# Kernel optimization log

Measured on AMD Instinct MI355X. Metric: run time of the kernel, lower is better.

## Reference

```python
import jax, jax.numpy as jnp
import numpy as np

B = 65536
N_PTS = 11        # n_trajectory_points
N_NEWTON = 5      # shooting_max_iter (fixed-count Newton shooting)
METRIC_FLOOR = 0.1


def _metric(c, lam, W1, b1, W2, b2, W3, b3):
    # g(c, lambda) > 0 ; c, lam: [B]
    x = jnp.stack([c, lam], axis=-1)              # [B, 2]
    h = jnp.tanh(x @ W1 + b1)
    h = jnp.tanh(h @ W2 + b2)
    return jax.nn.softplus((h @ W3 + b3)[..., 0]) + METRIC_FLOOR


def _christoffel(c, lam, mp):
    # 1-D manifold: Gamma = 0.5 * (dg/dc) / g  (dg/dc via forward-mode jvp)
    g, dg = jax.jvp(lambda cc: _metric(cc, lam, *mp), (c,), (jnp.ones_like(c),))
    return 0.5 * dg / g


def _integrate(c0, v0, lam, mp, n_pts):
    # RK4 integration of geodesic ODE  c' = v, v' = -Gamma(c) v^2  on t in [0,1]
    dt = 1.0 / (n_pts - 1)

    def deriv(c, v):
        return v, -_christoffel(c, lam, mp) * v * v

    def step(carry, _):
        c, v = carry
        k1c, k1v = deriv(c, v)
        k2c, k2v = deriv(c + 0.5 * dt * k1c, v + 0.5 * dt * k1v)
        k3c, k3v = deriv(c + 0.5 * dt * k2c, v + 0.5 * dt * k2v)
        k4c, k4v = deriv(c + dt * k3c, v + dt * k3v)
        cn = c + (dt / 6.0) * (k1c + 2 * k2c + 2 * k3c + k4c)
        vn = v + (dt / 6.0) * (k1v + 2 * k2v + 2 * k3v + k4v)
        return (cn, vn), (cn, vn)

    (cf, vf), (cs, vs) = jax.lax.scan(step, (c0, v0), None, length=n_pts - 1)
    cs = jnp.concatenate([c0[None], cs], axis=0)   # [T, B]
    vs = jnp.concatenate([v0[None], vs], axis=0)   # [T, B]
    traj = jnp.stack([cs, vs], axis=-1)            # [T, B, 2]
    return cf, jnp.transpose(traj, (1, 0, 2))      # final c [B], traj [B, T, 2]


def _shoot(c0, c1, lam, mp, n_pts):
    # Batched Newton shooting on initial velocity so that c(1) == c1.
    def final_c(v0):
        return _integrate(c0, v0, lam, mp, n_pts)[0]

    def newton(v0, _):
        out, dr = jax.jvp(final_c, (v0,), (jnp.ones_like(v0),))
        dr_safe = jnp.where(jnp.abs(dr) < 1e-6, 1e-6, dr)
        return v0 - (out - c1) / dr_safe, None

    v0, _ = jax.lax.scan(newton, c1 - c0, None, length=N_NEWTON)
    return v0


def setup_inputs() -> dict:
    key = jax.random.key(0)
    ks = jax.random.split(key, 8)
    f32 = jnp.float32
    return {
        "c_source": jax.random.uniform(ks[0], (B,), dtype=f32),
        "c_target": jax.random.uniform(ks[1], (B,), dtype=f32),
        "wavelength": jax.random.uniform(ks[2], (B,), dtype=f32),
        "W1": jax.random.normal(ks[3], (2, 16), dtype=f32) * 0.5,
        "b1": jnp.zeros((16,), f32),
        "W2": jax.random.normal(ks[4], (16, 16), dtype=f32) * 0.25,
        "b2": jnp.zeros((16,), f32),
        "W3": jax.random.normal(ks[5], (16, 1), dtype=f32) * 0.25,
        "b3": jnp.zeros((1,), f32),
        "D1": jax.random.normal(ks[6], (6, 64), dtype=f32) * 0.4,
        "d1": jnp.zeros((64,), f32),
        "D2": jax.random.normal(ks[7], (64, 1), dtype=f32) * 0.125,
        "d2": jnp.zeros((1,), f32),
    }


def reference(c_source, c_target, wavelength,
              W1, b1, W2, b2, W3, b3, D1, d1, D2, d2):
    mp = (W1, b1, W2, b2, W3, b3)
    # Vectorized geodesic BVP for the whole batch (replaces the Python loop)
    v0 = _shoot(c_source, c_target, wavelength, mp, N_PTS)
    _, traj = _integrate(c_source, v0, wavelength, mp, N_PTS)  # [B, T, 2]

    # AbsorbanceDecoder: path statistics + wavelength -> MLP -> absorbance
    c = traj[..., 0]
    v = traj[..., 1]
    path_len = jnp.sum(jnp.abs(jnp.diff(c, axis=1)), axis=1)
    feats = jnp.stack([c.mean(axis=1), c[:, -1], path_len,
                       v.mean(axis=1), jnp.abs(v).max(axis=1),
                       wavelength], axis=-1)                   # [B, 6]
    h = jnp.tanh(feats @ D1 + d1)
    absorbance = (h @ D2 + d2)[..., 0]                         # [B]
    return absorbance
```

## Files before the change

### kernel.cpp

```cpp
#include <hip/hip_runtime.h>
#include <math.h>

#define NPTS 11
#define METRIC_FLOOR 0.1f

#define RAWN 32
#define RAW2 1024
#define NG 30
#define SCALE_G 27.0f
#define INV_SCALE (1.0f / 27.0f)

#define WS_S  0
#define WS_SP 1024

typedef float v2f __attribute__((ext_vector_type(2)));

#define L2E 1.44269504088896340736f
#define LN2 0.69314718055994530942f

struct MW {
    float w1c[16], w1l[16], b1v[16], b2v[16], w3v[16];
};

static __device__ __forceinline__ float fast_tanh(float x) {
    float e = __builtin_amdgcn_exp2f(x * (2.0f * L2E));
    return fmaf(-2.0f, __builtin_amdgcn_rcpf(e + 1.0f), 1.0f);
}

extern "C" __global__ void table_raw_kernel(
    const float* __restrict__ W1, const float* __restrict__ b1,
    const float* __restrict__ W2, const float* __restrict__ b2,
    const float* __restrict__ W3, const float* __restrict__ b3,
    float* __restrict__ ws)
{
    __shared__ __align__(16) float sW2[256];
    const int t = threadIdx.x;
    sW2[t] = W2[t];
    __syncthreads();

    const int p = blockIdx.x * 256 + t;
    if (p >= RAW2) return;

    MW mw;
#pragma unroll
    for (int j = 0; j < 16; ++j) {
        mw.w1c[j] = W1[j];
        mw.w1l[j] = W1[16 + j];
        mw.b1v[j] = b1[j];
        mw.b2v[j] = b2[j];
        mw.w3v[j] = W3[j];
    }
    const float b3v = b3[0];

    const int ri = p & (RAWN - 1), rj = p >> 5;
    const float c   = (float)(ri - 2) * INV_SCALE;
    const float lam = (float)(rj - 2) * INV_SCALE;

    float h1[16], p1[16];
#pragma unroll
    for (int k = 0; k < 16; ++k) {
        float a  = mw.w1c[k];
        float u  = fmaf(c, a, fmaf(lam, mw.w1l[k], mw.b1v[k]));
        float t0 = fast_tanh(u);
        float s  = fmaf(-t0, t0, 1.0f);
        h1[k] = t0;
        p1[k] = s * a;
    }
    v2f U[8], DU[8];
#pragma unroll
    for (int jp = 0; jp < 8; ++jp) {
        U[jp]  = (v2f){mw.b2v[2*jp], mw.b2v[2*jp+1]};
        DU[jp] = (v2f){0.0f, 0.0f};
    }
#pragma unroll 2
    for (int i2 = 0; i2 < 16; ++i2) {
        const float4* wrow4 = reinterpret_cast<const float4*>(sW2 + i2 * 16);
        v2f hh = (v2f){h1[i2], h1[i2]};
        v2f pp = (v2f){p1[i2], p1[i2]};
#pragma unroll
        for (int q4 = 0; q4 < 4; ++q4) {
            float4 w4 = wrow4[q4];
            v2f wa = (v2f){w4.x, w4.y};
            v2f wb = (v2f){w4.z, w4.w};
            int jp = 2 * q4;
            U[jp]    = __builtin_elementwise_fma(wa, hh, U[jp]);
            DU[jp]   = __builtin_elementwise_fma(wa, pp, DU[jp]);
            U[jp+1]  = __builtin_elementwise_fma(wb, hh, U[jp+1]);
            DU[jp+1] = __builtin_elementwise_fma(wb, pp, DU[jp+1]);
        }
    }
    float z = b3v, dz = 0.0f;
#pragma unroll
    for (int jp = 0; jp < 8; ++jp)
#pragma unroll
        for (int k = 0; k < 2; ++k) {
            float u  = U[jp][k];
            float du = DU[jp][k];
            float t0 = fast_tanh(u);
            float s  = fmaf(-t0, t0, 1.0f);
            float w3 = mw.w3v[2*jp+k];
            z  = fmaf(t0, w3, z);
            dz = fmaf(s * du, w3, dz);
        }
    float az  = fabsf(z);
    float em  = __builtin_amdgcn_exp2f(-az * L2E);
    float r1  = __builtin_amdgcn_rcpf(1.0f + em);
    float spv = fmaxf(z, 0.0f) + __builtin_amdgcn_logf(1.0f + em) * LN2;
    float sig = (z >= 0.0f) ? r1 : (1.0f - r1);
    float g   = spv + METRIC_FLOOR;
    float dg  = sig * dz;

    float s  = sqrtf(g);
    ws[WS_S  + p] = s;
    ws[WS_SP + p] = 0.5f * dg * __builtin_amdgcn_rcpf(s);
}

static __device__ __forceinline__ void feval(
    const float4* __restrict__ r0, const float4* __restrict__ r1,
    float hy0, float hy1, float hy2, float hy3, float X,
    float& F_out, float& d_out)
{
    float fx = floorf(X);
    fx = fminf(fmaxf(fx, 0.0f), (float)(NG - 2));
    float tx = X - fx;
    int i0 = (int)fx;
    float t2 = tx * tx, t3 = t2 * tx;
    float h00 = fmaf(2.0f, t3, fmaf(-3.0f, t2, 1.0f));
    float h10 = t3 - 2.0f * t2 + tx;
    float h01 = fmaf(-2.0f, t3, 3.0f * t2);
    float h11 = t3 - t2;
    float d00 = 6.0f * (t2 - tx);
    float d10 = fmaf(3.0f, t2, fmaf(-4.0f, tx, 1.0f));
    float d01 = -d00;
    float d11 = fmaf(3.0f, t2, -2.0f * tx);

    float4 a0 = r0[i0], b0 = r0[i0 + 1];
    float4 a1 = r1[i0], b1 = r1[i0 + 1];
    const float h = INV_SCALE;

    float Fc0  = fmaf(h00, a0.x, fmaf(h10, h * a0.y, fmaf(h01, b0.x, h11 * (h * b0.y))));
    float dF0  = fmaf(d00, a0.x, fmaf(d10, h * a0.y, fmaf(d01, b0.x, d11 * (h * b0.y))));
    float FY0  = fmaf(h00, a0.z, fmaf(h10, h * a0.w, fmaf(h01, b0.z, h11 * (h * b0.w))));
    float dFY0 = fmaf(d00, a0.z, fmaf(d10, h * a0.w, fmaf(d01, b0.z, d11 * (h * b0.w))));
    float Fc1  = fmaf(h00, a1.x, fmaf(h10, h * a1.y, fmaf(h01, b1.x, h11 * (h * b1.y))));
    float dF1  = fmaf(d00, a1.x, fmaf(d10, h * a1.y, fmaf(d01, b1.x, d11 * (h * b1.y))));
    float FY1  = fmaf(h00, a1.z, fmaf(h10, h * a1.w, fmaf(h01, b1.z, h11 * (h * b1.w))));
    float dFY1 = fmaf(d00, a1.z, fmaf(d10, h * a1.w, fmaf(d01, b1.z, d11 * (h * b1.w))));

    F_out = fmaf(hy0, Fc0, fmaf(hy1, FY0, fmaf(hy2, Fc1, hy3 * FY1)));
    d_out = fmaf(hy0, dF0, fmaf(hy1, dFY0, fmaf(hy2, dF1, hy3 * dFY1)));
}

extern "C" __global__ __launch_bounds__(256, 1)
void geodesic_kernel(const float* __restrict__ gc0, const float* __restrict__ gc1,
                     const float* __restrict__ glam,
                     const float* __restrict__ D1, const float* __restrict__ d1,
                     const float* __restrict__ D2, const float* __restrict__ d2,
                     const float* __restrict__ ws,
                     float* __restrict__ out, int n)
{
    __shared__ __align__(16) float  ls[RAW2];
    __shared__ __align__(16) float  lsp[RAW2];
    __shared__ __align__(16) float  lF[RAW2];
    __shared__ __align__(16) float4 sH[NG * NG];
    __shared__ __align__(16) float  sD1[6 * 64];
    __shared__ __align__(16) float  sd1[64];
    __shared__ __align__(16) float  sD2[64];

    const int t = threadIdx.x;

    {
        const float4* wsS4  = reinterpret_cast<const float4*>(ws + WS_S);
        const float4* wsSP4 = reinterpret_cast<const float4*>(ws + WS_SP);
        const float4* D1f   = reinterpret_cast<const float4*>(D1);
        const float4* d1f   = reinterpret_cast<const float4*>(d1);
        const float4* D2f   = reinterpret_cast<const float4*>(D2);

        float4 sv  = wsS4[t];
        float4 spv = wsSP4[t];
        float4 tail_d = make_float4(0.f, 0.f, 0.f, 0.f);
        if (t < 128) tail_d = (t < 96) ? D1f[t]
                             : (t < 112 ? d1f[t - 96] : D2f[t - 112]);

        reinterpret_cast<float4*>(ls)[t]  = sv;
        reinterpret_cast<float4*>(lsp)[t] = spv;
        if (t < 128) {
            if (t < 96)       reinterpret_cast<float4*>(sD1)[t]       = tail_d;
            else if (t < 112) reinterpret_cast<float4*>(sd1)[t - 96]  = tail_d;
            else              reinterpret_cast<float4*>(sD2)[t - 112] = tail_d;
        }
    }
    __syncthreads();

    {
        const float h  = INV_SCALE;
        const float h2 = h * h * (1.0f / 12.0f);
#pragma unroll
        for (int k = 0; k < 4; ++k) {
            const int p = t + k * 256;
            const int col = p & (RAWN - 1);
            float s  = ls[p];
            float sp = lsp[p];
            float s_prev  = __shfl_up(s, 1, 32);
            float sp_prev = __shfl_up(sp, 1, 32);
            float F = (col == 0) ? 0.0f
                    : 0.5f * h * (s_prev + s) + h2 * (sp_prev - sp);
#pragma unroll
            for (int d = 1; d < 32; d <<= 1) {
                float o = __shfl_up(F, (unsigned)d, 32);
                if (col >= d) F += o;
            }
            lF[p] = F;
        }
    }
    __syncthreads();

    for (int p = t; p < NG * NG; p += 256) {
        const int ii = p % NG, jj = p / NG;
        const int ri = ii + 1, rj = jj + 1;
        float Fv = lF[rj * RAWN + ri];
        float sv = ls[rj * RAWN + ri];
        float FY = 0.5f * (lF[(rj + 1) * RAWN + ri] - lF[(rj - 1) * RAWN + ri]);
        float sY = 0.5f * (ls[(rj + 1) * RAWN + ri] - ls[(rj - 1) * RAWN + ri]);
        sH[p] = make_float4(Fv, sv, FY, sY);
    }
    __syncthreads();

    const int idx = blockIdx.x * blockDim.x + t;
    if (idx >= n) return;

    const float d2v = d2[0];
    const float c0  = gc0[idx];
    const float c1  = gc1[idx];
    const float lam = glam[idx];

    float sy = fmaf(lam, SCALE_G, 1.0f);
    float fy = fminf(fmaxf(floorf(sy), 0.0f), (float)(NG - 2));
    float ty = sy - fy;
    int j0 = (int)fy;
    float ty2 = ty * ty, ty3 = ty2 * ty;
    const float hy0 = fmaf(2.0f, ty3, fmaf(-3.0f, ty2, 1.0f));
    const float hy1 = ty3 - 2.0f * ty2 + ty;
    const float hy2 = fmaf(-2.0f, ty3, 3.0f * ty2);
    const float hy3 = ty3 - ty2;
    const float4* gr0 = sH + j0 * NG;
    const float4* gr1 = gr0 + NG;

    const float X0 = fmaf(c0, SCALE_G, 1.0f);
    const float X1 = fmaf(c1, SCALE_G, 1.0f);
    float F0, dd0, F1, dd1;
    feval(gr0, gr1, hy0, hy1, hy2, hy3, X0, F0, dd0);
    feval(gr0, gr1, hy0, hy1, hy2, hy3, X1, F1, dd1);
    const float L = F1 - F0;

    float X[9], dlast[9];
#pragma unroll
    for (int i = 0; i < 9; ++i)
        X[i] = fmaf((float)(i + 1) * 0.1f, X1 - X0, X0);
#pragma unroll
    for (int it = 0; it < 3; ++it) {
#pragma unroll
        for (int i = 0; i < 9; ++i) {
            float F, d;
            feval(gr0, gr1, hy0, hy1, hy2, hy3, X[i], F, d);
            float Ti = fmaf((float)(i + 1) * 0.1f, L, F0);
            X[i] -= (F - Ti) * __builtin_amdgcn_rcpf(d);
            dlast[i] = d;
        }
    }

    const float Lh = L * INV_SCALE;
    float csum = c0 + c1;
    float r0e = __builtin_amdgcn_rcpf(dd0);
    float r1e = __builtin_amdgcn_rcpf(dd1);
    float rsum = r0e + r1e;
    float rmax = fmaxf(r0e, r1e);
#pragma unroll
    for (int i = 0; i < 9; ++i) {
        csum += (X[i] - 1.0f) * INV_SCALE;
        float r = __builtin_amdgcn_rcpf(dlast[i]);
        rsum += r;
        rmax = fmaxf(rmax, r);
    }
    const float vsum = Lh * rsum;
    const float vmax = fabsf(Lh) * rmax;
    const float plen = fabsf(c1 - c0);

    const float inv_npts = 1.0f / (float)NPTS;
    const float f0 = csum * inv_npts;
    const float f1 = c1;
    const float f2 = plen;
    const float f3 = vsum * inv_npts;
    const float f4 = vmax;
    const float f5 = lam;

    float acc = d2v;
#pragma unroll 4
    for (int j = 0; j < 64; ++j) {
        float u = sd1[j];
        u = fmaf(f0, sD1[0 * 64 + j], u);
        u = fmaf(f1, sD1[1 * 64 + j], u);
        u = fmaf(f2, sD1[2 * 64 + j], u);
        u = fmaf(f3, sD1[3 * 64 + j], u);
        u = fmaf(f4, sD1[4 * 64 + j], u);
        u = fmaf(f5, sD1[5 * 64 + j], u);
        acc = fmaf(fast_tanh(u), sD2[j], acc);
    }
    out[idx] = acc;
}

extern "C" void kernel_launch(void* const* d_in, const int* in_sizes, int n_in,
                              void* d_out, int out_size, void* d_ws, size_t ws_size,
                              hipStream_t stream) {
    const float* c_source   = (const float*)d_in[0];
    const float* c_target   = (const float*)d_in[1];
    const float* wavelength = (const float*)d_in[2];
    const float* W1 = (const float*)d_in[3];
    const float* b1 = (const float*)d_in[4];
    const float* W2 = (const float*)d_in[5];
    const float* b2 = (const float*)d_in[6];
    const float* W3 = (const float*)d_in[7];
    const float* b3 = (const float*)d_in[8];
    const float* D1 = (const float*)d_in[9];
    const float* d1 = (const float*)d_in[10];
    const float* D2 = (const float*)d_in[11];
    const float* d2 = (const float*)d_in[12];
    float* out = (float*)d_out;
    float* ws  = (float*)d_ws;

    const int n = in_sizes[0];

    hipLaunchKernelGGL(table_raw_kernel, dim3(RAW2 / 256), dim3(256), 0,
                       stream, W1, b1, W2, b2, W3, b3, ws);

    const int block = 256;
    const int grid  = (n + block - 1) / block;
    hipLaunchKernelGGL(geodesic_kernel, dim3(grid), dim3(block), 0, stream,
                       c_source, c_target, wavelength,
                       D1, d1, D2, d2, ws, out, n);
}
```

Before: 19.57 us.

## Fuse metric table build into geodesic kernel, drop derivative via 4th-order quadrature

Removes the separate table-building kernel launch and its global workspace round-trip. Each block now evaluates the metric MLP on the 32x32 grid itself, and the derivative path (dg/dc) is gone. The cumulative integral uses a fourth-order stencil from neighbouring s values instead of an endpoint-corrected trapezoid that needed s'. This saves a launch and global traffic, but every one of the 256 blocks recomputes the 1024-point MLP table (4 evaluations per thread), which adds redundant compute before the main work.

After: 21.19 us. +8.3%, slower.

```diff
diff --git a/kernel.cpp b/kernel.cpp
--- a/kernel.cpp
+++ b/kernel.cpp
@@ -10,9 +10,6 @@
 #define SCALE_G 27.0f
 #define INV_SCALE (1.0f / 27.0f)
 
-#define WS_S  0
-#define WS_SP 1024
-
 typedef float v2f __attribute__((ext_vector_type(2)));
 
 #define L2E 1.44269504088896340736f
@@ -27,92 +24,39 @@
     return fmaf(-2.0f, __builtin_amdgcn_rcpf(e + 1.0f), 1.0f);
 }
 
-extern "C" __global__ void table_raw_kernel(
-    const float* __restrict__ W1, const float* __restrict__ b1,
-    const float* __restrict__ W2, const float* __restrict__ b2,
-    const float* __restrict__ W3, const float* __restrict__ b3,
-    float* __restrict__ ws)
+static __device__ __forceinline__ float metric_s(
+    float c, float lam, const MW& mw, const float* __restrict__ sW2, float b3v)
 {
-    __shared__ __align__(16) float sW2[256];
-    const int t = threadIdx.x;
-    sW2[t] = W2[t];
-    __syncthreads();
-
-    const int p = blockIdx.x * 256 + t;
-    if (p >= RAW2) return;
-
-    MW mw;
+    float h1[16];
 #pragma unroll
     for (int j = 0; j < 16; ++j) {
-        mw.w1c[j] = W1[j];
-        mw.w1l[j] = W1[16 + j];
-        mw.b1v[j] = b1[j];
-        mw.b2v[j] = b2[j];
-        mw.w3v[j] = W3[j];
-    }
-    const float b3v = b3[0];
-
-    const int ri = p & (RAWN - 1), rj = p >> 5;
-    const float c   = (float)(ri - 2) * INV_SCALE;
-    const float lam = (float)(rj - 2) * INV_SCALE;
-
-    float h1[16], p1[16];
-#pragma unroll
-    for (int k = 0; k < 16; ++k) {
-        float a  = mw.w1c[k];
-        float u  = fmaf(c, a, fmaf(lam, mw.w1l[k], mw.b1v[k]));
-        float t0 = fast_tanh(u);
-        float s  = fmaf(-t0, t0, 1.0f);
-        h1[k] = t0;
-        p1[k] = s * a;
-    }
-    v2f U[8], DU[8];
-#pragma unroll
-    for (int jp = 0; jp < 8; ++jp) {
-        U[jp]  = (v2f){mw.b2v[2*jp], mw.b2v[2*jp+1]};
-        DU[jp] = (v2f){0.0f, 0.0f};
-    }
+        float u = fmaf(c, mw.w1c[j], fmaf(lam, mw.w1l[j], mw.b1v[j]));
+        h1[j] = fast_tanh(u);
+    }
+    v2f U[8];
+#pragma unroll
+    for (int jp = 0; jp < 8; ++jp) U[jp] = (v2f){mw.b2v[2*jp], mw.b2v[2*jp+1]};
 #pragma unroll 2
-    for (int i2 = 0; i2 < 16; ++i2) {
-        const float4* wrow4 = reinterpret_cast<const float4*>(sW2 + i2 * 16);
-        v2f hh = (v2f){h1[i2], h1[i2]};
-        v2f pp = (v2f){p1[i2], p1[i2]};
+    for (int i = 0; i < 16; ++i) {
+        const float4* wrow4 = reinterpret_cast<const float4*>(sW2 + i * 16);
+        v2f hh = (v2f){h1[i], h1[i]};
 #pragma unroll
         for (int q4 = 0; q4 < 4; ++q4) {
             float4 w4 = wrow4[q4];
-            v2f wa = (v2f){w4.x, w4.y};
-            v2f wb = (v2f){w4.z, w4.w};
-            int jp = 2 * q4;
-            U[jp]    = __builtin_elementwise_fma(wa, hh, U[jp]);
-            DU[jp]   = __builtin_elementwise_fma(wa, pp, DU[jp]);
-            U[jp+1]  = __builtin_elementwise_fma(wb, hh, U[jp+1]);
-            DU[jp+1] = __builtin_elementwise_fma(wb, pp, DU[jp+1]);
+            U[2*q4]   = __builtin_elementwise_fma((v2f){w4.x, w4.y}, hh, U[2*q4]);
+            U[2*q4+1] = __builtin_elementwise_fma((v2f){w4.z, w4.w}, hh, U[2*q4+1]);
         }
     }
-    float z = b3v, dz = 0.0f;
+    float z = b3v;
 #pragma unroll
     for (int jp = 0; jp < 8; ++jp)
 #pragma unroll
-        for (int k = 0; k < 2; ++k) {
-            float u  = U[jp][k];
-            float du = DU[jp][k];
-            float t0 = fast_tanh(u);
-            float s  = fmaf(-t0, t0, 1.0f);
-            float w3 = mw.w3v[2*jp+k];
-            z  = fmaf(t0, w3, z);
-            dz = fmaf(s * du, w3, dz);
-        }
-    float az  = fabsf(z);
-    float em  = __builtin_amdgcn_exp2f(-az * L2E);
-    float r1  = __builtin_amdgcn_rcpf(1.0f + em);
-    float spv = fmaxf(z, 0.0f) + __builtin_amdgcn_logf(1.0f + em) * LN2;
-    float sig = (z >= 0.0f) ? r1 : (1.0f - r1);
-    float g   = spv + METRIC_FLOOR;
-    float dg  = sig * dz;
-
-    float s  = sqrtf(g);
-    ws[WS_S  + p] = s;
-    ws[WS_SP + p] = 0.5f * dg * __builtin_amdgcn_rcpf(s);
+        for (int k = 0; k < 2; ++k)
+            z = fmaf(fast_tanh(U[jp][k]), mw.w3v[2*jp+k], z);
+    float az = fabsf(z);
+    float em = __builtin_amdgcn_exp2f(-az * L2E);
+    float sp = fmaxf(z, 0.0f) + __builtin_amdgcn_logf(1.0f + em) * LN2;
+    return sqrtf(sp + METRIC_FLOOR);
 }
 
 static __device__ __forceinline__ void feval(
@@ -154,13 +98,15 @@
 extern "C" __global__ __launch_bounds__(256, 1)
 void geodesic_kernel(const float* __restrict__ gc0, const float* __restrict__ gc1,
                      const float* __restrict__ glam,
+                     const float* __restrict__ W1, const float* __restrict__ b1,
+                     const float* __restrict__ W2, const float* __restrict__ b2,
+                     const float* __restrict__ W3, const float* __restrict__ b3,
                      const float* __restrict__ D1, const float* __restrict__ d1,
                      const float* __restrict__ D2, const float* __restrict__ d2,
-                     const float* __restrict__ ws,
                      float* __restrict__ out, int n)
 {
+    __shared__ __align__(16) float  sW2[256];
     __shared__ __align__(16) float  ls[RAW2];
-    __shared__ __align__(16) float  lsp[RAW2];
     __shared__ __align__(16) float  lF[RAW2];
     __shared__ __align__(16) float4 sH[NG * NG];
     __shared__ __align__(16) float  sD1[6 * 64];
@@ -169,42 +115,51 @@
 
     const int t = threadIdx.x;
 
+    sW2[t] = W2[t];
+    for (int i = t; i < 384; i += 256) sD1[i] = D1[i];
+    if (t < 64) sd1[t] = d1[t];
+    if (t >= 64 && t < 128) sD2[t - 64] = D2[t - 64];
+
+    MW mw;
+#pragma unroll
+    for (int j = 0; j < 16; ++j) {
+        mw.w1c[j] = W1[j];
+        mw.w1l[j] = W1[16 + j];
+        mw.b1v[j] = b1[j];
+        mw.b2v[j] = b2[j];
+        mw.w3v[j] = W3[j];
+    }
+    const float b3v = b3[0];
+    const float d2v = d2[0];
+    __syncthreads();
+
+    float sv[4];
+#pragma unroll
+    for (int k = 0; k < 4; ++k) {
+        const int p  = t + k * 256;
+        const int ri = p & (RAWN - 1);
+        const int rj = p >> 5;
+        sv[k] = metric_s((float)(ri - 2) * INV_SCALE,
+                         (float)(rj - 2) * INV_SCALE, mw, sW2, b3v);
+        ls[p] = sv[k];
+    }
+
     {
-        const float4* wsS4  = reinterpret_cast<const float4*>(ws + WS_S);
-        const float4* wsSP4 = reinterpret_cast<const float4*>(ws + WS_SP);
-        const float4* D1f   = reinterpret_cast<const float4*>(D1);
-        const float4* d1f   = reinterpret_cast<const float4*>(d1);
-        const float4* D2f   = reinterpret_cast<const float4*>(D2);
-
-        float4 sv  = wsS4[t];
-        float4 spv = wsSP4[t];
-        float4 tail_d = make_float4(0.f, 0.f, 0.f, 0.f);
-        if (t < 128) tail_d = (t < 96) ? D1f[t]
-                             : (t < 112 ? d1f[t - 96] : D2f[t - 112]);
-
-        reinterpret_cast<float4*>(ls)[t]  = sv;
-        reinterpret_cast<float4*>(lsp)[t] = spv;
-        if (t < 128) {
-            if (t < 96)       reinterpret_cast<float4*>(sD1)[t]       = tail_d;
-            else if (t < 112) reinterpret_cast<float4*>(sd1)[t - 96]  = tail_d;
-            else              reinterpret_cast<float4*>(sD2)[t - 112] = tail_d;
-        }
-    }
-    __syncthreads();
-
-    {
-        const float h  = INV_SCALE;
-        const float h2 = h * h * (1.0f / 12.0f);
+        const float h = INV_SCALE;
 #pragma unroll
         for (int k = 0; k < 4; ++k) {
-            const int p = t + k * 256;
+            const int p   = t + k * 256;
             const int col = p & (RAWN - 1);
-            float s  = ls[p];
-            float sp = lsp[p];
-            float s_prev  = __shfl_up(s, 1, 32);
-            float sp_prev = __shfl_up(sp, 1, 32);
-            float F = (col == 0) ? 0.0f
-                    : 0.5f * h * (s_prev + s) + h2 * (sp_prev - sp);
+            float s   = sv[k];
+            float sm1 = __shfl_up(s, 1, 32);
+            float sm2 = __shfl_up(s, 2, 32);
+            float sp1 = __shfl_down(s, 1, 32);
+            float inc;
+            if (col == 0)        inc = 0.0f;
+            else if (col == 1)   inc = h * (5.0f * sm1 + 8.0f * s - sp1) * (1.0f / 12.0f);
+            else if (col == 31)  inc = h * (-sm2 + 8.0f * sm1 + 5.0f * s) * (1.0f / 12.0f);
+            else                 inc = h * (13.0f * (sm1 + s) - sm2 - sp1) * (1.0f / 24.0f);
+            float F = inc;
 #pragma unroll
             for (int d = 1; d < 32; d <<= 1) {
                 float o = __shfl_up(F, (unsigned)d, 32);
@@ -219,17 +174,16 @@
         const int ii = p % NG, jj = p / NG;
         const int ri = ii + 1, rj = jj + 1;
         float Fv = lF[rj * RAWN + ri];
-        float sv = ls[rj * RAWN + ri];
+        float sq = ls[rj * RAWN + ri];
         float FY = 0.5f * (lF[(rj + 1) * RAWN + ri] - lF[(rj - 1) * RAWN + ri]);
         float sY = 0.5f * (ls[(rj + 1) * RAWN + ri] - ls[(rj - 1) * RAWN + ri]);
-        sH[p] = make_float4(Fv, sv, FY, sY);
+        sH[p] = make_float4(Fv, sq, FY, sY);
     }
     __syncthreads();
 
     const int idx = blockIdx.x * blockDim.x + t;
     if (idx >= n) return;
 
-    const float d2v = d2[0];
     const float c0  = gc0[idx];
     const float c1  = gc1[idx];
     const float lam = glam[idx];
@@ -326,16 +280,11 @@
     const float* D2 = (const float*)d_in[11];
     const float* d2 = (const float*)d_in[12];
     float* out = (float*)d_out;
-    float* ws  = (float*)d_ws;
 
     const int n = in_sizes[0];
-
-    hipLaunchKernelGGL(table_raw_kernel, dim3(RAW2 / 256), dim3(256), 0,
-                       stream, W1, b1, W2, b2, W3, b3, ws);
-
     const int block = 256;
     const int grid  = (n + block - 1) / block;
     hipLaunchKernelGGL(geodesic_kernel, dim3(grid), dim3(block), 0, stream,
                        c_source, c_target, wavelength,
-                       D1, d1, D2, d2, ws, out, n);
-}
+                       W1, b1, W2, b2, W3, b3, D1, d1, D2, d2, out, n);
+}
```
